# Performance work log

Hardware: AMD Instinct MI355X
Metric: run time of the kernel (lower is better)

Reference implementation:

```python
import jax, jax.numpy as jnp
import numpy as np

N_HEADS = 6
N_KV_HEADS = 2
HEAD_DIM = 128
REPEATS = N_HEADS // N_KV_HEADS  # 3


def setup_inputs() -> dict:
    key = jax.random.key(0)
    ks = jax.random.split(key, 5)
    B, S, D = 2, 4096, 768
    std = 1.0 / np.sqrt(D)
    return {
        "x": jax.random.normal(ks[0], (B, S, D), dtype=jnp.float32),
        "wq": jax.random.normal(ks[1], (D, N_HEADS * HEAD_DIM), dtype=jnp.float32) * std,
        "wk": jax.random.normal(ks[2], (D, N_KV_HEADS * HEAD_DIM), dtype=jnp.float32) * std,
        "wv": jax.random.normal(ks[3], (D, N_KV_HEADS * HEAD_DIM), dtype=jnp.float32) * std,
        "wo": jax.random.normal(ks[4], (N_HEADS * HEAD_DIM, D), dtype=jnp.float32) * std,
    }


def reference(x, wq, wk, wv, wo):
    B, S, _ = x.shape
    # projections
    q = (x @ wq).reshape(B, S, N_HEADS, HEAD_DIM)
    k = (x @ wk).reshape(B, S, N_KV_HEADS, HEAD_DIM)
    v = (x @ wv).reshape(B, S, N_KV_HEADS, HEAD_DIM)
    # GQA: repeat kv heads (repeat_interleave along head axis)
    k = jnp.repeat(k, REPEATS, axis=2)  # [B,S,H,D]
    v = jnp.repeat(v, REPEATS, axis=2)
    scale = 1.0 / jnp.sqrt(jnp.asarray(HEAD_DIM, x.dtype))
    # full bidirectional attention, [B,H,S,S] scores
    attn = jnp.einsum("bqhd,bkhd->bhqk", q * scale, k)
    attn = jax.nn.softmax(attn, axis=-1)
    out = jnp.einsum("bhqk,bkhd->bqhd", attn, v).reshape(B, S, N_HEADS * HEAD_DIM)
    return out @ wo
```

## Files before the change

### kernel.cpp

```cpp
#include <hip/hip_runtime.h>


typedef __attribute__((ext_vector_type(8))) short bf16x8;
typedef __attribute__((ext_vector_type(4))) float floatx4;
typedef __attribute__((ext_vector_type(4))) unsigned short ushort4v;

#define MFMA16(a, b, c) __builtin_amdgcn_mfma_f32_16x16x32_bf16((a), (b), (c), 0, 0, 0)

#if __has_builtin(__builtin_amdgcn_exp2f)
#define EXP2F(x) __builtin_amdgcn_exp2f(x)
#else
#define EXP2F(x) exp2f(x)
#endif

#define GLOAD_LDS16(gptr, lptr)                                                   \
  __builtin_amdgcn_global_load_lds(                                               \
      (const __attribute__((address_space(1))) unsigned int*)(gptr),              \
      (__attribute__((address_space(3))) unsigned int*)(lptr), 16, 0, 0)

__device__ __forceinline__ unsigned short f2bf(float f) {
  unsigned int u = __builtin_bit_cast(unsigned int, f);
  u = u + 0x7FFFu + ((u >> 16) & 1u);
  return (unsigned short)(u >> 16);
}

__device__ __forceinline__ unsigned short f2bf_fast(float f) {
  unsigned int u = __builtin_bit_cast(unsigned int, f);
  return (unsigned short)((u + 0x8000u) >> 16);
}

__device__ __forceinline__ float bf2f(unsigned short v) {
  return __builtin_bit_cast(float, (unsigned int)v << 16);
}


__global__ __launch_bounds__(256) void k_cvt_x(const float* __restrict__ x,
                                               unsigned short* __restrict__ xb, int n) {
  int i = (blockIdx.x * 256 + threadIdx.x) * 4;
  if (i + 3 < n) {
    float4 v = *(const float4*)(x + i);
    xb[i + 0] = f2bf(v.x);
    xb[i + 1] = f2bf(v.y);
    xb[i + 2] = f2bf(v.z);
    xb[i + 3] = f2bf(v.w);
  }
}

__global__ __launch_bounds__(256) void k_cvt_w(const float* __restrict__ wq,
                                               const float* __restrict__ wk,
                                               const float* __restrict__ wv,
                                               const float* __restrict__ wo,
                                               unsigned short* __restrict__ wqkvT,
                                               unsigned short* __restrict__ woT) {
  __shared__ float T[64 * 65];
  const float QSCALE = 1.4426950408889634f * 0.08838834764831843f;
  const int kb = blockIdx.x, nb = blockIdx.y, tid = threadIdx.x;

  const float* src; int ld, col0; unsigned short* dst; int n0; float scale = 1.0f;
  if (nb < 12)      { src = wq; ld = 768; col0 = nb * 64;        dst = wqkvT; n0 = nb * 64; scale = QSCALE; }
  else if (nb < 16) { src = wk; ld = 256; col0 = (nb - 12) * 64; dst = wqkvT; n0 = nb * 64; }
  else if (nb < 20) { src = wv; ld = 256; col0 = (nb - 16) * 64; dst = wqkvT; n0 = nb * 64; }
  else              { src = wo; ld = 768; col0 = (nb - 20) * 64; dst = woT;   n0 = (nb - 20) * 64; }

  const int k0 = kb * 64;
  {
    int cc = tid & 63, kk0 = tid >> 6;
#pragma unroll
    for (int it = 0; it < 16; it++) {
      int kk = kk0 + it * 4;
      T[kk * 65 + cc] = src[(size_t)(k0 + kk) * ld + col0 + cc] * scale;
    }
  }
  __syncthreads();
  {
    int kk = tid & 63, nn0 = tid >> 6;
#pragma unroll
    for (int it = 0; it < 16; it++) {
      int nn = nn0 + it * 4;
      dst[(size_t)(n0 + nn) * 768 + k0 + kk] = f2bf(T[kk * 65 + nn]);
    }
  }
}


__device__ __forceinline__ void store_out(float* C, int i, float v) { C[i] = v; }
__device__ __forceinline__ void store_out(unsigned short* C, int i, float v) { C[i] = f2bf(v); }

template <typename OUT_T, bool SPLIT_V>
__global__ __launch_bounds__(256) void k_gemm(const unsigned short* __restrict__ A, int lda,
                                              const unsigned short* __restrict__ Bt, int ldb,
                                              OUT_T* __restrict__ C, int ldc, int K,
                                              unsigned short* __restrict__ vTout) {
  __shared__ __align__(16) unsigned short As0[128 * 32];
  __shared__ __align__(16) unsigned short As1[128 * 32];
  __shared__ __align__(16) unsigned short Bs0[128 * 32];
  __shared__ __align__(16) unsigned short Bs1[128 * 32];

  const int tid = threadIdx.x;
  const int wave = tid >> 6, lane = tid & 63;
  const int quad = lane >> 4, l16 = lane & 15;
  const int wm = (wave >> 1) * 64, wn = (wave & 1) * 64;
  const int m0 = blockIdx.y * 128, n0 = blockIdx.x * 128;

  floatx4 acc[4][4] = {};

  auto stage = [&](const unsigned short* G, int ld, int row0, int k0, unsigned short* S) {
#pragma unroll
    for (int it = 0; it < 2; it++) {
      int j = it * 256 + tid;
      int r = j >> 2, c = (j & 3) ^ (r & 3);
      GLOAD_LDS16((const char*)(G + (size_t)(row0 + r) * ld + k0 + c * 8), &S[j * 8]);
    }
  };

  const int xq = (quad ^ (l16 & 3)) * 8;
  auto compute = [&](const unsigned short* As, const unsigned short* Bs) {
    bf16x8 af[4], bfr[4];
#pragma unroll
    for (int mf = 0; mf < 4; mf++)
      af[mf] = *(const bf16x8*)(&As[(wm + mf * 16 + l16) * 32 + xq]);
#pragma unroll
    for (int nf = 0; nf < 4; nf++)
      bfr[nf] = *(const bf16x8*)(&Bs[(wn + nf * 16 + l16) * 32 + xq]);
#pragma unroll
    for (int mf = 0; mf < 4; mf++)
#pragma unroll
      for (int nf = 0; nf < 4; nf++)
        acc[mf][nf] = MFMA16(af[mf], bfr[nf], acc[mf][nf]);
  };

  stage(A, lda, m0, 0, As0);
  stage(Bt, ldb, n0, 0, Bs0);

  const int half = K >> 6;
#pragma unroll 1
  for (int i = 0; i < half; i++) {
    __syncthreads();
    stage(A, lda, m0, (2 * i + 1) * 32, As1);
    stage(Bt, ldb, n0, (2 * i + 1) * 32, Bs1);
    compute(As0, Bs0);
    __syncthreads();
    if (i < half - 1) {
      stage(A, lda, m0, (2 * i + 2) * 32, As0);
      stage(Bt, ldb, n0, (2 * i + 2) * 32, Bs0);
    }
    compute(As1, Bs1);
  }

#pragma unroll
  for (int mf = 0; mf < 4; mf++)
#pragma unroll
    for (int nf = 0; nf < 4; nf++) {
      int col = n0 + wn + nf * 16 + l16;
      if (SPLIT_V && col >= 1024) {
        int cc = col - 1024;
        int kvhh = cc >> 7, d = cc & 127;
        int row0 = m0 + wm + mf * 16 + quad * 4;
        int bb = row0 >> 12, s = row0 & 4095;
        ushort4v pv;
        pv.x = f2bf(acc[mf][nf][0]);
        pv.y = f2bf(acc[mf][nf][1]);
        pv.z = f2bf(acc[mf][nf][2]);
        pv.w = f2bf(acc[mf][nf][3]);
        *(ushort4v*)(&vTout[((size_t)((bb * 2 + kvhh) * 128) + d) * 4096 + s]) = pv;
      } else {
#pragma unroll
        for (int r = 0; r < 4; r++) {
          int row = m0 + wm + mf * 16 + quad * 4 + r;
          store_out(C, row * ldc + col, acc[mf][nf][r]);
        }
      }
    }
}


#define NSEG 4

#define KS_OFF(row, c) (((row) << 7) + ((((c) ^ ((row) & 7))) << 3))
#define VS_OFF(row, c) (((row) << 6) + ((((c) ^ ((row) & 7))) << 3))

__global__ __launch_bounds__(256, 3) void k_attn(const unsigned short* __restrict__ qkv,
                                                 const unsigned short* __restrict__ vT,
                                                 unsigned short* __restrict__ Opart,
                                                 float* __restrict__ lpart) {
  __shared__ __align__(16) unsigned short Ks[64 * 128];
  __shared__ __align__(16) unsigned short Vt[128 * 64];
  __shared__ __align__(16) unsigned short Ps[128 * 64];

  const int qt = blockIdx.x, h = blockIdx.y;
  const int seg = blockIdx.z >> 1, b = blockIdx.z & 1;
  const int kvh = h / 3;
  const int tid = threadIdx.x, w = tid >> 6, lane = tid & 63;
  const int quad = lane >> 4, l16 = lane & 15;

  const char* qbase = (const char*)(qkv + (size_t)(b * 4096) * 1280 + h * 128);
  const char* kbase = (const char*)(qkv + (size_t)(b * 4096) * 1280 + 768 + kvh * 128);
  const char* vtb   = (const char*)(vT + (size_t)((b * 2 + kvh) * 128) * 4096);

  bf16x8 qf[2][4];
  floatx4 acc[2][8] = {};
  float l_i[2] = {0.f, 0.f};

#pragma unroll
  for (int it = 0; it < 8; it++) {
    int cb = it * 256 + w * 64;
    int j = cb + lane;
    int r = j >> 4, c = (j & 15) ^ (r & 7);
    unsigned short* dst = (cb < 1024) ? &Ks[cb * 8] : &Vt[(cb - 1024) * 8];
    GLOAD_LDS16(qbase + (size_t)(qt * 128 + r) * 2560 + c * 16, dst);
  }
  __syncthreads();

  {
    const unsigned short* qsrc = (w < 2) ? Ks : Vt;
    const int qr0 = (w & 1) * 32;
#pragma unroll
    for (int qg = 0; qg < 2; qg++)
#pragma unroll
      for (int dc = 0; dc < 4; dc++)
        qf[qg][dc] = *(const bf16x8*)(&qsrc[KS_OFF(qr0 + qg * 16 + l16, dc * 4 + quad)]);
  }
  __syncthreads();

  auto stage_k = [&](int kt) {
#pragma unroll
    for (int it = 0; it < 4; it++) {
      int cb = it * 256 + w * 64;
      int j = cb + lane;
      int r = j >> 4, c = (j & 15) ^ (r & 7);
      GLOAD_LDS16(kbase + (size_t)(kt * 64 + r) * 2560 + c * 16, &Ks[cb * 8]);
    }
  };
  auto stage_v = [&](int kt) {
#pragma unroll
    for (int it = 0; it < 4; it++) {
      int cb = it * 256 + w * 64;
      int j = cb + lane;
      int r = j >> 3, c = (j & 7) ^ (r & 7);
      GLOAD_LDS16(vtb + (size_t)r * 8192 + kt * 128 + c * 16, &Vt[cb * 8]);
    }
  };

  const int k0 = seg * 16;
  stage_k(k0);

#pragma unroll 1
  for (int i = 0; i < 16; i++) {
    __syncthreads();
    stage_v(k0 + i);

    floatx4 sfr[2][4] = {};
#pragma unroll
    for (int nf = 0; nf < 4; nf++)
#pragma unroll
      for (int dc = 0; dc < 4; dc++) {
        bf16x8 kf = *(const bf16x8*)(&Ks[KS_OFF(nf * 16 + l16, dc * 4 + quad)]);
        sfr[0][nf] = MFMA16(kf, qf[0][dc], sfr[0][nf]);
        sfr[1][nf] = MFMA16(kf, qf[1][dc], sfr[1][nf]);
      }

#pragma unroll
    for (int qg = 0; qg < 2; qg++) {
      float rs = 0.f;
#pragma unroll
      for (int nf = 0; nf < 4; nf++) {
#pragma unroll
        for (int r = 0; r < 4; r++) {
          float p = EXP2F(sfr[qg][nf][r]);
          sfr[qg][nf][r] = p;
          rs += p;
        }
        int row = w * 32 + qg * 16 + l16;
        int ch = nf * 2 + (quad >> 1);
        ushort4v pw;
        pw.x = f2bf_fast(sfr[qg][nf][0]);
        pw.y = f2bf_fast(sfr[qg][nf][1]);
        pw.z = f2bf_fast(sfr[qg][nf][2]);
        pw.w = f2bf_fast(sfr[qg][nf][3]);
        *(ushort4v*)(&Ps[VS_OFF(row, ch) + (quad & 1) * 4]) = pw;
      }
      l_i[qg] += rs;
    }

    __syncthreads();
    if (i < 15) stage_k(k0 + i + 1);

#pragma unroll
    for (int kc = 0; kc < 2; kc++) {
      bf16x8 pf0 = *(const bf16x8*)(&Ps[VS_OFF(w * 32 + l16, kc * 4 + quad)]);
      bf16x8 pf1 = *(const bf16x8*)(&Ps[VS_OFF(w * 32 + 16 + l16, kc * 4 + quad)]);
#pragma unroll
      for (int df = 0; df < 8; df++) {
        bf16x8 vf = *(const bf16x8*)(&Vt[VS_OFF(df * 16 + l16, kc * 4 + quad)]);
        acc[0][df] = MFMA16(pf0, vf, acc[0][df]);
        acc[1][df] = MFMA16(pf1, vf, acc[1][df]);
      }
    }
  }

#pragma unroll
  for (int qg = 0; qg < 2; qg++) {
    float lt = l_i[qg];
    lt += __shfl_xor(lt, 16, 64);
    lt += __shfl_xor(lt, 32, 64);
    if (quad == 0)
      lpart[((size_t)(seg * 2 + b) * 6 + h) * 4096 + qt * 128 + w * 32 + qg * 16 + l16] = lt;
#pragma unroll
    for (int r = 0; r < 4; r++) {
      int row = qt * 128 + w * 32 + qg * 16 + quad * 4 + r;
      unsigned short* orow =
          Opart + (size_t)seg * 8192 * 768 + (size_t)(b * 4096 + row) * 768 + h * 128;
#pragma unroll
      for (int df = 0; df < 8; df++)
        orow[df * 16 + l16] = f2bf_fast(acc[qg][df][r]);
    }
  }
}

__global__ __launch_bounds__(256) void k_reduce(const unsigned short* __restrict__ Opart,
                                                const float* __restrict__ lpart,
                                                unsigned short* __restrict__ ob) {
  int idx = (blockIdx.x * 256 + threadIdx.x) * 4;
  int row = idx / 768, col = idx - row * 768;
  int h = col >> 7;
  int b = row >> 12, r = row & 4095;

  float lt = 0.f;
#pragma unroll
  for (int s = 0; s < NSEG; s++)
    lt += lpart[((size_t)(s * 2 + b) * 6 + h) * 4096 + r];
  float inv = 1.0f / lt;

  float acc0 = 0.f, acc1 = 0.f, acc2 = 0.f, acc3 = 0.f;
#pragma unroll
  for (int s = 0; s < NSEG; s++) {
    ushort4v v = *(const ushort4v*)(&Opart[(size_t)s * 8192 * 768 + idx]);
    acc0 += bf2f(v.x);
    acc1 += bf2f(v.y);
    acc2 += bf2f(v.z);
    acc3 += bf2f(v.w);
  }
  ushort4v o;
  o.x = f2bf(acc0 * inv);
  o.y = f2bf(acc1 * inv);
  o.z = f2bf(acc2 * inv);
  o.w = f2bf(acc3 * inv);
  *(ushort4v*)(&ob[idx]) = o;
}


extern "C" void kernel_launch(void* const* d_in, const int* in_sizes, int n_in,
                              void* d_out, int out_size, void* d_ws, size_t ws_size,
                              hipStream_t stream) {
  const float* x  = (const float*)d_in[0];
  const float* wq = (const float*)d_in[1];
  const float* wk = (const float*)d_in[2];
  const float* wv = (const float*)d_in[3];
  const float* wo = (const float*)d_in[4];
  float* out = (float*)d_out;

  char* ws = (char*)d_ws;
  unsigned short* xb    = (unsigned short*)(ws);
  unsigned short* wqkvT = (unsigned short*)(ws + 12582912);
  unsigned short* woT   = (unsigned short*)(ws + 14548992);
  unsigned short* qkvb  = (unsigned short*)(ws + 15728640);
  unsigned short* ob    = (unsigned short*)(ws + 36700160);
  unsigned short* Opart = (unsigned short*)(ws + 49283072);
  float*          lpart = (float*)(ws + 99614720);
  unsigned short* vT    = ob;

  k_cvt_x<<<6144, 256, 0, stream>>>(x, xb, 8192 * 768);
  k_cvt_w<<<dim3(12, 32), 256, 0, stream>>>(wq, wk, wv, wo, wqkvT, woT);

  k_gemm<unsigned short, true><<<dim3(10, 64), 256, 0, stream>>>(
      xb, 768, wqkvT, 768, qkvb, 1280, 768, vT);

  k_attn<<<dim3(32, 6, 2 * NSEG), 256, 0, stream>>>(qkvb, vT, Opart, lpart);

  k_reduce<<<6144, 256, 0, stream>>>(Opart, lpart, ob);

  k_gemm<float, false><<<dim3(6, 64), 256, 0, stream>>>(ob, 768, woT, 768, out, 768, 768, nullptr);
}
```

Before: 310.6 us.

## Use 8 waves per attention block with 16 query rows each

Doubles the attention block to 512 threads, so each wave handles 16 query rows instead of 32. Per-thread register use drops, since the Q fragments, score tiles and output accumulators are halved, and staging loads are spread over more waves. The cost is that each K/V fragment read from LDS now feeds one MFMA instead of two, which doubles LDS read traffic per FLOP.

```diff
diff --git a/kernel.cpp b/kernel.cpp
--- a/kernel.cpp
+++ b/kernel.cpp
@@ -179,7 +179,7 @@
 #define KS_OFF(row, c) (((row) << 7) + ((((c) ^ ((row) & 7))) << 3))
 #define VS_OFF(row, c) (((row) << 6) + ((((c) ^ ((row) & 7))) << 3))
 
-__global__ __launch_bounds__(256, 3) void k_attn(const unsigned short* __restrict__ qkv,
+__global__ __launch_bounds__(512, 4) void k_attn(const unsigned short* __restrict__ qkv,
                                                  const unsigned short* __restrict__ vT,
                                                  unsigned short* __restrict__ Opart,
                                                  float* __restrict__ lpart) {
@@ -197,13 +197,13 @@
   const char* kbase = (const char*)(qkv + (size_t)(b * 4096) * 1280 + 768 + kvh * 128);
   const char* vtb   = (const char*)(vT + (size_t)((b * 2 + kvh) * 128) * 4096);
 
-  bf16x8 qf[2][4];
-  floatx4 acc[2][8] = {};
-  float l_i[2] = {0.f, 0.f};
-
-#pragma unroll
-  for (int it = 0; it < 8; it++) {
-    int cb = it * 256 + w * 64;
+  bf16x8 qf[4];
+  floatx4 acc[8] = {};
+  float l_i = 0.f;
+
+#pragma unroll
+  for (int it = 0; it < 4; it++) {
+    int cb = it * 512 + w * 64;
     int j = cb + lane;
     int r = j >> 4, c = (j & 15) ^ (r & 7);
     unsigned short* dst = (cb < 1024) ? &Ks[cb * 8] : &Vt[(cb - 1024) * 8];
@@ -212,20 +212,18 @@
   __syncthreads();
 
   {
-    const unsigned short* qsrc = (w < 2) ? Ks : Vt;
-    const int qr0 = (w & 1) * 32;
-#pragma unroll
-    for (int qg = 0; qg < 2; qg++)
-#pragma unroll
-      for (int dc = 0; dc < 4; dc++)
-        qf[qg][dc] = *(const bf16x8*)(&qsrc[KS_OFF(qr0 + qg * 16 + l16, dc * 4 + quad)]);
+    const unsigned short* qsrc = (w < 4) ? Ks : Vt;
+    const int qr0 = (w & 3) * 16;
+#pragma unroll
+    for (int dc = 0; dc < 4; dc++)
+      qf[dc] = *(const bf16x8*)(&qsrc[KS_OFF(qr0 + l16, dc * 4 + quad)]);
   }
   __syncthreads();
 
   auto stage_k = [&](int kt) {
 #pragma unroll
-    for (int it = 0; it < 4; it++) {
-      int cb = it * 256 + w * 64;
+    for (int it = 0; it < 2; it++) {
+      int cb = it * 512 + w * 64;
       int j = cb + lane;
       int r = j >> 4, c = (j & 15) ^ (r & 7);
       GLOAD_LDS16(kbase + (size_t)(kt * 64 + r) * 2560 + c * 16, &Ks[cb * 8]);
@@ -233,8 +231,8 @@
   };
   auto stage_v = [&](int kt) {
 #pragma unroll
-    for (int it = 0; it < 4; it++) {
-      int cb = it * 256 + w * 64;
+    for (int it = 0; it < 2; it++) {
+      int cb = it * 512 + w * 64;
       int j = cb + lane;
       int r = j >> 3, c = (j & 7) ^ (r & 7);
       GLOAD_LDS16(vtb + (size_t)r * 8192 + kt * 128 + c * 16, &Vt[cb * 8]);
@@ -249,37 +247,35 @@
     __syncthreads();
     stage_v(k0 + i);
 
-    floatx4 sfr[2][4] = {};
+    floatx4 sfr[4] = {};
 #pragma unroll
     for (int nf = 0; nf < 4; nf++)
 #pragma unroll
       for (int dc = 0; dc < 4; dc++) {
         bf16x8 kf = *(const bf16x8*)(&Ks[KS_OFF(nf * 16 + l16, dc * 4 + quad)]);
-        sfr[0][nf] = MFMA16(kf, qf[0][dc], sfr[0][nf]);
-        sfr[1][nf] = MFMA16(kf, qf[1][dc], sfr[1][nf]);
+        sfr[nf] = MFMA16(kf, qf[dc], sfr[nf]);
       }
 
-#pragma unroll
-    for (int qg = 0; qg < 2; qg++) {
+    {
       float rs = 0.f;
 #pragma unroll
       for (int nf = 0; nf < 4; nf++) {
 #pragma unroll
         for (int r = 0; r < 4; r++) {
-          float p = EXP2F(sfr[qg][nf][r]);
-          sfr[qg][nf][r] = p;
+          float p = EXP2F(sfr[nf][r]);
+          sfr[nf][r] = p;
           rs += p;
         }
-        int row = w * 32 + qg * 16 + l16;
+        int row = w * 16 + l16;
         int ch = nf * 2 + (quad >> 1);
         ushort4v pw;
-        pw.x = f2bf_fast(sfr[qg][nf][0]);
-        pw.y = f2bf_fast(sfr[qg][nf][1]);
-        pw.z = f2bf_fast(sfr[qg][nf][2]);
-        pw.w = f2bf_fast(sfr[qg][nf][3]);
+        pw.x = f2bf_fast(sfr[nf][0]);
+        pw.y = f2bf_fast(sfr[nf][1]);
+        pw.z = f2bf_fast(sfr[nf][2]);
+        pw.w = f2bf_fast(sfr[nf][3]);
         *(ushort4v*)(&Ps[VS_OFF(row, ch) + (quad & 1) * 4]) = pw;
       }
-      l_i[qg] += rs;
+      l_i += rs;
     }
 
     __syncthreads();
@@ -287,32 +283,29 @@
 
 #pragma unroll
     for (int kc = 0; kc < 2; kc++) {
-      bf16x8 pf0 = *(const bf16x8*)(&Ps[VS_OFF(w * 32 + l16, kc * 4 + quad)]);
-      bf16x8 pf1 = *(const bf16x8*)(&Ps[VS_OFF(w * 32 + 16 + l16, kc * 4 + quad)]);
+      bf16x8 pf = *(const bf16x8*)(&Ps[VS_OFF(w * 16 + l16, kc * 4 + quad)]);
 #pragma unroll
       for (int df = 0; df < 8; df++) {
         bf16x8 vf = *(const bf16x8*)(&Vt[VS_OFF(df * 16 + l16, kc * 4 + quad)]);
-        acc[0][df] = MFMA16(pf0, vf, acc[0][df]);
-        acc[1][df] = MFMA16(pf1, vf, acc[1][df]);
+        acc[df] = MFMA16(pf, vf, acc[df]);
       }
     }
   }
 
-#pragma unroll
-  for (int qg = 0; qg < 2; qg++) {
-    float lt = l_i[qg];
+  {
+    float lt = l_i;
     lt += __shfl_xor(lt, 16, 64);
     lt += __shfl_xor(lt, 32, 64);
     if (quad == 0)
-      lpart[((size_t)(seg * 2 + b) * 6 + h) * 4096 + qt * 128 + w * 32 + qg * 16 + l16] = lt;
+      lpart[((size_t)(seg * 2 + b) * 6 + h) * 4096 + qt * 128 + w * 16 + l16] = lt;
 #pragma unroll
     for (int r = 0; r < 4; r++) {
-      int row = qt * 128 + w * 32 + qg * 16 + quad * 4 + r;
+      int row = qt * 128 + w * 16 + quad * 4 + r;
       unsigned short* orow =
           Opart + (size_t)seg * 8192 * 768 + (size_t)(b * 4096 + row) * 768 + h * 128;
 #pragma unroll
       for (int df = 0; df < 8; df++)
-        orow[df * 16 + l16] = f2bf_fast(acc[qg][df][r]);
+        orow[df * 16 + l16] = f2bf_fast(acc[df][r]);
     }
   }
 }
@@ -375,7 +368,7 @@
   k_gemm<unsigned short, true><<<dim3(10, 64), 256, 0, stream>>>(
       xb, 768, wqkvT, 768, qkvb, 1280, 768, vT);
 
-  k_attn<<<dim3(32, 6, 2 * NSEG), 256, 0, stream>>>(qkvb, vT, Opart, lpart);
+  k_attn<<<dim3(32, 6, 2 * NSEG), 512, 0, stream>>>(qkvb, vT, Opart, lpart);
 
   k_reduce<<<6144, 256, 0, stream>>>(Opart, lpart, ob);
 
```

After: 264.7 us. 1.17x faster.

## Double-buffer K and V tiles in attention with one barrier per iteration

Applied to the files above, without the earlier changes.

The attention kernel now keeps two LDS buffers each for the K and V tiles. The loads for tile i+1 are issued right after the barrier of iteration i, while tile i is being computed, and the second barrier per iteration is removed. This is meant to hide global-to-LDS latency and cut synchronisation cost. In exchange, LDS per block grows from about 48KB to 80KB and the launch_bounds occupancy hint of 3 is dropped, which may lower the number of resident blocks per CU.

```diff
diff --git a/kernel.cpp b/kernel.cpp
--- a/kernel.cpp
+++ b/kernel.cpp
@@ -179,12 +179,12 @@
 #define KS_OFF(row, c) (((row) << 7) + ((((c) ^ ((row) & 7))) << 3))
 #define VS_OFF(row, c) (((row) << 6) + ((((c) ^ ((row) & 7))) << 3))
 
-__global__ __launch_bounds__(256, 3) void k_attn(const unsigned short* __restrict__ qkv,
-                                                 const unsigned short* __restrict__ vT,
-                                                 unsigned short* __restrict__ Opart,
-                                                 float* __restrict__ lpart) {
-  __shared__ __align__(16) unsigned short Ks[64 * 128];
-  __shared__ __align__(16) unsigned short Vt[128 * 64];
+__global__ __launch_bounds__(256) void k_attn(const unsigned short* __restrict__ qkv,
+                                              const unsigned short* __restrict__ vT,
+                                              unsigned short* __restrict__ Opart,
+                                              float* __restrict__ lpart) {
+  __shared__ __align__(16) unsigned short Ks[2][64 * 128];
+  __shared__ __align__(16) unsigned short Vt[2][128 * 64];
   __shared__ __align__(16) unsigned short Ps[128 * 64];
 
   const int qt = blockIdx.x, h = blockIdx.y;
@@ -206,13 +206,13 @@
     int cb = it * 256 + w * 64;
     int j = cb + lane;
     int r = j >> 4, c = (j & 15) ^ (r & 7);
-    unsigned short* dst = (cb < 1024) ? &Ks[cb * 8] : &Vt[(cb - 1024) * 8];
+    unsigned short* dst = (cb < 1024) ? &Ks[0][cb * 8] : &Ks[1][(cb - 1024) * 8];
     GLOAD_LDS16(qbase + (size_t)(qt * 128 + r) * 2560 + c * 16, dst);
   }
   __syncthreads();
 
   {
-    const unsigned short* qsrc = (w < 2) ? Ks : Vt;
+    const unsigned short* qsrc = (w < 2) ? Ks[0] : Ks[1];
     const int qr0 = (w & 1) * 32;
 #pragma unroll
     for (int qg = 0; qg < 2; qg++)
@@ -222,39 +222,45 @@
   }
   __syncthreads();
 
-  auto stage_k = [&](int kt) {
+  auto stage_k = [&](int kt, unsigned short* dstKs) {
 #pragma unroll
     for (int it = 0; it < 4; it++) {
       int cb = it * 256 + w * 64;
       int j = cb + lane;
       int r = j >> 4, c = (j & 15) ^ (r & 7);
-      GLOAD_LDS16(kbase + (size_t)(kt * 64 + r) * 2560 + c * 16, &Ks[cb * 8]);
+      GLOAD_LDS16(kbase + (size_t)(kt * 64 + r) * 2560 + c * 16, &dstKs[cb * 8]);
     }
   };
-  auto stage_v = [&](int kt) {
+  auto stage_v = [&](int kt, unsigned short* dstVt) {
 #pragma unroll
     for (int it = 0; it < 4; it++) {
       int cb = it * 256 + w * 64;
       int j = cb + lane;
       int r = j >> 3, c = (j & 7) ^ (r & 7);
-      GLOAD_LDS16(vtb + (size_t)r * 8192 + kt * 128 + c * 16, &Vt[cb * 8]);
+      GLOAD_LDS16(vtb + (size_t)r * 8192 + kt * 128 + c * 16, &dstVt[cb * 8]);
     }
   };
 
   const int k0 = seg * 16;
-  stage_k(k0);
+  stage_k(k0, Ks[0]);
+  stage_v(k0, Vt[0]);
 
 #pragma unroll 1
   for (int i = 0; i < 16; i++) {
     __syncthreads();
-    stage_v(k0 + i);
+    if (i < 15) {
+      stage_k(k0 + i + 1, Ks[(i + 1) & 1]);
+      stage_v(k0 + i + 1, Vt[(i + 1) & 1]);
+    }
+    const unsigned short* Kc = Ks[i & 1];
+    const unsigned short* Vc = Vt[i & 1];
 
     floatx4 sfr[2][4] = {};
 #pragma unroll
     for (int nf = 0; nf < 4; nf++)
 #pragma unroll
       for (int dc = 0; dc < 4; dc++) {
-        bf16x8 kf = *(const bf16x8*)(&Ks[KS_OFF(nf * 16 + l16, dc * 4 + quad)]);
+        bf16x8 kf = *(const bf16x8*)(&Kc[KS_OFF(nf * 16 + l16, dc * 4 + quad)]);
         sfr[0][nf] = MFMA16(kf, qf[0][dc], sfr[0][nf]);
         sfr[1][nf] = MFMA16(kf, qf[1][dc], sfr[1][nf]);
       }
@@ -282,16 +288,13 @@
       l_i[qg] += rs;
     }
 
-    __syncthreads();
-    if (i < 15) stage_k(k0 + i + 1);
-
 #pragma unroll
     for (int kc = 0; kc < 2; kc++) {
       bf16x8 pf0 = *(const bf16x8*)(&Ps[VS_OFF(w * 32 + l16, kc * 4 + quad)]);
       bf16x8 pf1 = *(const bf16x8*)(&Ps[VS_OFF(w * 32 + 16 + l16, kc * 4 + quad)]);
 #pragma unroll
       for (int df = 0; df < 8; df++) {
-        bf16x8 vf = *(const bf16x8*)(&Vt[VS_OFF(df * 16 + l16, kc * 4 + quad)]);
+        bf16x8 vf = *(const bf16x8*)(&Vc[VS_OFF(df * 16 + l16, kc * 4 + quad)]);
         acc[0][df] = MFMA16(pf0, vf, acc[0][df]);
         acc[1][df] = MFMA16(pf1, vf, acc[1][df]);
       }
```

Result: faster. 271.0 us (-12.7%).
